# Optimization experiments

Measured on AMD Instinct MI355X. Metric: run time of the kernel, lower is better.

The kernel has to match this reference:

```python
import jax, jax.numpy as jnp
import numpy as np

EPS = 1e-8
DIGIT_TEMPERATURE = 1.0
SEED = 0
B, KMAX, V = 64, 16, 32000
DV, H = 10, 4096
# permute_prob table: prob_table[k] = permute_prob.get(k, 0.0)
_PROB = np.zeros(KMAX + 1, dtype=np.float32)
_PROB[2:] = 0.5
PROB_TABLE = jnp.asarray(_PROB)


def setup_inputs() -> dict:
    key = jax.random.key(0)
    ks = jax.random.split(key, 6)
    p_raw = jax.random.uniform(ks[0], (B, KMAX, V), dtype=jnp.float32)
    p_z = p_raw / p_raw.sum(axis=-1, keepdims=True)  # valid distributions per slot
    return {
        "p_z": p_z,
        "digit_logits_ref": jax.random.normal(ks[1], (B, DV), dtype=jnp.float32),
        "digit_logits_cf": jax.random.normal(ks[2], (B, DV), dtype=jnp.float32),
        "h_ans_ref": jax.random.normal(ks[3], (B, H), dtype=jnp.float32),
        "h_ans_cf": jax.random.normal(ks[4], (B, H), dtype=jnp.float32),
        "k_vals": jax.random.randint(ks[5], (B,), 0, KMAX + 1),
    }


def _js_divergence(p, q, eps=EPS):
    p = jnp.clip(p.astype(jnp.float32), eps)
    q = jnp.clip(q.astype(jnp.float32), eps)
    m = 0.5 * (p + q)
    log_m = jnp.log(m)
    kl_pm = (p * (jnp.log(p) - log_m)).sum(-1)
    kl_qm = (q * (jnp.log(q) - log_m)).sum(-1)
    return 0.5 * (kl_pm + kl_qm)


def _build_counterfactual_pz(p_z, k_vals):
    # Vectorized GS-mode counterfactual: per batch, with prob permute_prob[k]
    # (and k>1) permute the first k slots, otherwise temperature-warp them.
    bsz, kmax, vocab = p_z.shape
    key = jax.random.key(SEED)
    k_dec, k_perm, k_tau = jax.random.split(key, 3)
    u_dec = jax.random.uniform(k_dec, (bsz,))
    do_permute = (k_vals > 1) & (u_dec < PROB_TABLE[k_vals])  # [B]
    slots = jnp.arange(kmax)
    active = slots[None, :] < k_vals[:, None]  # [B, K]
    # ragged permutation of the first k slots: argsort random keys, inactive -> +inf
    u_perm = jax.random.uniform(k_perm, (bsz, kmax))
    perm = jnp.argsort(jnp.where(active, u_perm, jnp.inf), axis=1)  # stable: tail keeps order
    permuted = jnp.take_along_axis(p_z, perm[:, :, None], axis=1)
    # temperature warp: softmax(log(p)/tau), tau ~ U(0.7, 1.6) per slot
    tau = jax.random.uniform(k_tau, (bsz, kmax, 1), minval=0.7, maxval=1.6)
    warped = jax.nn.softmax(jnp.log(jnp.clip(p_z, EPS)) / tau, axis=-1)
    cf = jnp.where(do_permute[:, None, None], permuted, warped)
    return jnp.where(active[:, :, None], cf, p_z)


def reference(p_z, digit_logits_ref, digit_logits_cf, h_ans_ref, h_ans_cf, k_vals):
    p_cf_z = _build_counterfactual_pz(p_z, k_vals)
    # safe_softmax(logits, tau) == softmax(logits / tau)
    p_ref = jax.lax.stop_gradient(
        jax.nn.softmax(digit_logits_ref / DIGIT_TEMPERATURE, axis=-1))
    p_cf = jax.nn.softmax(digit_logits_cf / DIGIT_TEMPERATURE, axis=-1)
    js = _js_divergence(p_ref, p_cf).mean()
    loss_cf = jnp.log(jnp.float32(2.0)) - js
    ref_f = jax.lax.stop_gradient(h_ans_ref.astype(jnp.float32))
    cf_f = h_ans_cf.astype(jnp.float32)
    ref_norm = ref_f / jnp.clip(jnp.linalg.norm(ref_f, axis=-1, keepdims=True), 1e-12)
    cf_norm = cf_f / jnp.clip(jnp.linalg.norm(cf_f, axis=-1, keepdims=True), 1e-12)
    cos_sim = (ref_norm * cf_norm).sum(-1).mean()
    loss_dep = cos_sim - 1.0  # cf_mode == 'gs'
    dep_norm = jnp.linalg.norm(ref_f - cf_f, axis=-1).mean()
    return loss_cf, loss_dep, dep_norm, p_cf_z
```

## Files before the change

kernel.cpp:

```cpp
#include <hip/hip_runtime.h>
#include <stdint.h>

#define NB    64
#define KMAX  16
#define VV    32000
#define DVV   10
#define HH    4096
#define NROWS (NB*KMAX)
#define EPSF  1e-8f
#define NQ    8000

__device__ __forceinline__ uint32_t rotl32(uint32_t v, int r) { return (v << r) | (v >> (32 - r)); }

__device__ __forceinline__ void tf2x32(uint32_t k0, uint32_t k1, uint32_t c0, uint32_t c1,
                                       uint32_t& o0, uint32_t& o1) {
    uint32_t ks2 = k0 ^ k1 ^ 0x1BD11BDAu;
    uint32_t x0 = c0 + k0, x1 = c1 + k1;
    const int RA[4] = {13, 15, 26, 6};
    const int RB[4] = {17, 29, 16, 24};
#pragma unroll
    for (int i = 0; i < 4; ++i) { x0 += x1; x1 = rotl32(x1, RA[i]); x1 ^= x0; }
    x0 += k1; x1 += ks2 + 1u;
#pragma unroll
    for (int i = 0; i < 4; ++i) { x0 += x1; x1 = rotl32(x1, RB[i]); x1 ^= x0; }
    x0 += ks2; x1 += k0 + 2u;
#pragma unroll
    for (int i = 0; i < 4; ++i) { x0 += x1; x1 = rotl32(x1, RA[i]); x1 ^= x0; }
    x0 += k0; x1 += k1 + 3u;
#pragma unroll
    for (int i = 0; i < 4; ++i) { x0 += x1; x1 = rotl32(x1, RB[i]); x1 ^= x0; }
    x0 += k1; x1 += ks2 + 4u;
#pragma unroll
    for (int i = 0; i < 4; ++i) { x0 += x1; x1 = rotl32(x1, RA[i]); x1 ^= x0; }
    x0 += ks2; x1 += k0 + 5u;
    o0 = x0; o1 = x1;
}

__device__ __forceinline__ float bits_to_u01(uint32_t bits) {
    uint32_t fb = (bits >> 9) | 0x3F800000u;
    return __uint_as_float(fb) - 1.0f;
}

__global__ __launch_bounds__(1024) void setup_kernel(const int* __restrict__ k_vals,
                                                     int* __restrict__ src_arr,
                                                     float* __restrict__ itau_arr) {
    const int j = threadIdx.x;
    const int b = j >> 4, s = j & 15;

    __shared__ float su[NROWS];
    __shared__ int   sk[NB];
    __shared__ int   sdp[NB];

    uint32_t a0, b0, a1, b1, a2, b2;
    tf2x32(0u, 0u, 0u, 3u, a0, b0);
    tf2x32(0u, 0u, 1u, 4u, a1, b1);
    tf2x32(0u, 0u, 2u, 5u, a2, b2);
    const uint32_t kdec0 = a0, kdec1 = a1;
    const uint32_t kperm0 = a2, kperm1 = b0;
    const uint32_t ktau0 = b1, ktau1 = b2;

    uint32_t y0, y1, pb, tb;
    if (j < 512) { tf2x32(kperm0, kperm1, (uint32_t)j, (uint32_t)(j + 512), y0, y1); pb = y0; }
    else         { tf2x32(kperm0, kperm1, (uint32_t)(j - 512), (uint32_t)j, y0, y1); pb = y1; }
    su[j] = bits_to_u01(pb);
    if (j < 512) { tf2x32(ktau0, ktau1, (uint32_t)j, (uint32_t)(j + 512), y0, y1); tb = y0; }
    else         { tf2x32(ktau0, ktau1, (uint32_t)(j - 512), (uint32_t)j, y0, y1); tb = y1; }
    float tau = fmaxf(0.7f, bits_to_u01(tb) * 0.9f + 0.7f);
    float itau = 1.0f / tau;

    if (j < NB) {
        uint32_t bits;
        if (j < 32) { tf2x32(kdec0, kdec1, (uint32_t)j, (uint32_t)(j + 32), y0, y1); bits = y0; }
        else        { tf2x32(kdec0, kdec1, (uint32_t)(j - 32), (uint32_t)j, y0, y1); bits = y1; }
        float u_dec = bits_to_u01(bits);
        int k = k_vals[j];
        float prob = (k >= 2) ? 0.5f : 0.0f;
        sk[j] = k;
        sdp[j] = (k > 1) && (u_dec < prob);
    }
    __syncthreads();

    const int k = sk[b];
    const bool dp = sdp[b] != 0;
    const float INF = __int_as_float(0x7F800000);
    const float myk = (s < k) ? su[j] : INF;

    int r = 0;
#pragma unroll
    for (int t = 0; t < KMAX; ++t) {
        float kt = (t < k) ? su[(b << 4) + t] : INF;
        r += (kt < myk) || (kt == myk && t < s);
    }

    if (s >= k)      { src_arr[j] = s;            itau_arr[j] = 0.0f; }
    else if (dp)     { src_arr[(b << 4) + r] = s; itau_arr[(b << 4) + r] = 0.0f; }
    else             { src_arr[j] = -1;           itau_arr[j] = itau; }
}

__global__ __launch_bounds__(256) void rowred_kernel(const float* __restrict__ hr,
                                                     const float* __restrict__ hc,
                                                     float* __restrict__ cosb,
                                                     float* __restrict__ depb) {
    int b = blockIdx.x;
    const float4* r4 = (const float4*)(hr + (size_t)b * HH);
    const float4* c4 = (const float4*)(hc + (size_t)b * HH);
    float srr = 0.f, scc = 0.f, sxc = 0.f, sdd = 0.f;
    for (int i = threadIdx.x; i < HH / 4; i += 256) {
        float4 r = r4[i], c = c4[i];
        srr += r.x * r.x + r.y * r.y + r.z * r.z + r.w * r.w;
        scc += c.x * c.x + c.y * c.y + c.z * c.z + c.w * c.w;
        sxc += r.x * c.x + r.y * c.y + r.z * c.z + r.w * c.w;
        float dx = r.x - c.x, dy = r.y - c.y, dz = r.z - c.z, dw = r.w - c.w;
        sdd += dx * dx + dy * dy + dz * dz + dw * dw;
    }
#pragma unroll
    for (int o = 32; o; o >>= 1) {
        srr += __shfl_down(srr, o, 64);
        scc += __shfl_down(scc, o, 64);
        sxc += __shfl_down(sxc, o, 64);
        sdd += __shfl_down(sdd, o, 64);
    }
    __shared__ float red[4][4];
    int w = threadIdx.x >> 6;
    if ((threadIdx.x & 63) == 0) { red[w][0] = srr; red[w][1] = scc; red[w][2] = sxc; red[w][3] = sdd; }
    __syncthreads();
    if (threadIdx.x == 0) {
        float t0 = 0.f, t1 = 0.f, t2 = 0.f, t3 = 0.f;
        for (int i = 0; i < 4; ++i) { t0 += red[i][0]; t1 += red[i][1]; t2 += red[i][2]; t3 += red[i][3]; }
        float nr = fmaxf(sqrtf(t0), 1e-12f);
        float nc = fmaxf(sqrtf(t1), 1e-12f);
        cosb[b] = t2 / (nr * nc);
        depb[b] = sqrtf(t3);
    }
}

__global__ void finalize_kernel(const float* __restrict__ dlr, const float* __restrict__ dlc,
                                const float* __restrict__ cosb, const float* __restrict__ depb,
                                float* __restrict__ out) {
    int b = threadIdx.x;
    float lr[DVV], lc[DVV];
    float mr = -1e30f, mc = -1e30f;
#pragma unroll
    for (int v = 0; v < DVV; ++v) {
        lr[v] = dlr[b * DVV + v]; lc[v] = dlc[b * DVV + v];
        mr = fmaxf(mr, lr[v]); mc = fmaxf(mc, lc[v]);
    }
    float sr = 0.f, sc = 0.f;
#pragma unroll
    for (int v = 0; v < DVV; ++v) {
        lr[v] = expf(lr[v] - mr); sr += lr[v];
        lc[v] = expf(lc[v] - mc); sc += lc[v];
    }
    float js = 0.f;
#pragma unroll
    for (int v = 0; v < DVV; ++v) {
        float p = fmaxf(lr[v] / sr, EPSF);
        float q = fmaxf(lc[v] / sc, EPSF);
        float m = 0.5f * (p + q);
        float lm = logf(m);
        js += 0.5f * (p * (logf(p) - lm) + q * (logf(q) - lm));
    }
    float cs = cosb[b], dp = depb[b];
#pragma unroll
    for (int o = 32; o; o >>= 1) {
        js += __shfl_down(js, o, 64);
        cs += __shfl_down(cs, o, 64);
        dp += __shfl_down(dp, o, 64);
    }
    if (b == 0) {
        out[0] = logf(2.0f) - js * (1.0f / 64.0f);
        out[1] = cs * (1.0f / 64.0f) - 1.0f;
        out[2] = dp * (1.0f / 64.0f);
    }
}

__global__ __launch_bounds__(1024) void cf_main_kernel(const float* __restrict__ p_z,
                                                       const int* __restrict__ src_arr,
                                                       const float* __restrict__ itau_arr,
                                                       float* __restrict__ out) {
    const int row = blockIdx.x;
    const int b = row >> 4;
    const int src = src_arr[row];
    const int tid = threadIdx.x;
    const int lane = tid & 63;
    float* dst = out + (size_t)row * VV;

    if (src >= 0) {
        const float* s = p_z + ((size_t)((b << 4) + src)) * VV;
#pragma unroll
        for (int i = 0; i < 8; ++i) {
            const int q = tid + (i << 10);
            if (q >= NQ) break;
            float4 v = *(const float4*)(s + (q << 2));
            float nx = __shfl_down(v.x, 1, 64);
            if (q < NQ - 1) {
                float4 st;
                st.x = v.y; st.y = v.z; st.z = v.w;
                st.w = (lane == 63) ? s[(q << 2) + 4] : nx;
                *(float4*)(dst + (q << 2) + 1) = st;
            }
            if (q == 0) dst[0] = v.x;
            if (q == NQ - 1) { dst[VV - 3] = v.y; dst[VV - 2] = v.z; dst[VV - 1] = v.w; }
        }
        return;
    }

    const float it = itau_arr[row];
    const float* s = p_z + (size_t)row * VV;
    float4 r[8];
    float lsum = 0.f;
#pragma unroll
    for (int i = 0; i < 8; ++i) {
        const int q = tid + (i << 10);
        if (q < NQ) {
            float4 v = *(const float4*)(s + (q << 2));
            v.x = exp2f(__log2f(fmaxf(v.x, EPSF)) * it);
            v.y = exp2f(__log2f(fmaxf(v.y, EPSF)) * it);
            v.z = exp2f(__log2f(fmaxf(v.z, EPSF)) * it);
            v.w = exp2f(__log2f(fmaxf(v.w, EPSF)) * it);
            r[i] = v;
            lsum += v.x + v.y + v.z + v.w;
        } else {
            r[i] = make_float4(0.f, 0.f, 0.f, 0.f);
        }
    }
    __shared__ float red[16];
    float t = lsum;
#pragma unroll
    for (int o = 32; o; o >>= 1) t += __shfl_down(t, o, 64);
    if (lane == 0) red[tid >> 6] = t;
    __syncthreads();
    if (tid < 64) {
        float u = (tid < 16) ? red[tid] : 0.0f;
#pragma unroll
        for (int o = 8; o; o >>= 1) u += __shfl_down(u, o, 64);
        if (tid == 0) red[0] = u;
    }
    __syncthreads();
    const float scale = 1.0f / red[0];

#pragma unroll
    for (int i = 0; i < 8; ++i) {
        const int q = tid + (i << 10);
        if (q >= NQ) break;
        float nx = __shfl_down(r[i].x, 1, 64);
        if (q < NQ - 1) {
            float4 st;
            st.x = r[i].y * scale; st.y = r[i].z * scale; st.z = r[i].w * scale;
            if (lane == 63)
                nx = exp2f(__log2f(fmaxf(s[(q << 2) + 4], EPSF)) * it);
            st.w = nx * scale;
            *(float4*)(dst + (q << 2) + 1) = st;
        }
        if (q == 0) dst[0] = r[i].x * scale;
        if (q == NQ - 1) {
            dst[VV - 3] = r[i].y * scale;
            dst[VV - 2] = r[i].z * scale;
            dst[VV - 1] = r[i].w * scale;
        }
    }
}

extern "C" void kernel_launch(void* const* d_in, const int* in_sizes, int n_in,
                              void* d_out, int out_size, void* d_ws, size_t ws_size,
                              hipStream_t stream) {
    const float* p_z = (const float*)d_in[0];
    const float* dlr = (const float*)d_in[1];
    const float* dlc = (const float*)d_in[2];
    const float* hr  = (const float*)d_in[3];
    const float* hc  = (const float*)d_in[4];
    const int*   kv  = (const int*)d_in[5];
    float* out = (float*)d_out;

    int*   src_arr  = (int*)d_ws;
    float* itau_arr = (float*)d_ws + NROWS;
    float* cosb     = (float*)d_ws + 2 * NROWS;
    float* depb     = cosb + NB;

    setup_kernel<<<1, 1024, 0, stream>>>(kv, src_arr, itau_arr);
    cf_main_kernel<<<NROWS, 1024, 0, stream>>>(p_z, src_arr, itau_arr, out + 3);
    rowred_kernel<<<NB, 256, 0, stream>>>(hr, hc, cosb, depb);
    finalize_kernel<<<1, 64, 0, stream>>>(dlr, dlc, cosb, depb, out);
}
```

Measured before the change: 62.64 us.

## Split warp normalization into row-sum pass and flat grid-stride output kernel

Replaces the one-block-per-row counterfactual kernel with two kernels. The first computes the per-row softmax normalization for warped rows. The second is a flat grid-stride kernel that writes aligned float4 stores across the whole output, with offsets handled per element group. This removes the shuffles and register-held rows of the old kernel and gives an even, row-independent workload. The cost is reading warped rows twice and doing a per-group integer division and extra branching.

```diff
diff --git a/kernel.cpp b/kernel.cpp
--- a/kernel.cpp
+++ b/kernel.cpp
@@ -9,6 +9,8 @@
 #define NROWS (NB*KMAX)
 #define EPSF  1e-8f
 #define NQ    8000
+#define TOTELEM (NROWS*VV)
+#define TGROUPS ((TOTELEM - 4) / 4)
 
 __device__ __forceinline__ uint32_t rotl32(uint32_t v, int r) { return (v << r) | (v >> (32 - r)); }
 
@@ -95,6 +97,84 @@
     if (s >= k)      { src_arr[j] = s;            itau_arr[j] = 0.0f; }
     else if (dp)     { src_arr[(b << 4) + r] = s; itau_arr[(b << 4) + r] = 0.0f; }
     else             { src_arr[j] = -1;           itau_arr[j] = itau; }
+}
+
+__global__ __launch_bounds__(256) void rowsum_kernel(const float* __restrict__ p_z,
+                                                     const int* __restrict__ src_arr,
+                                                     const float* __restrict__ itau_arr,
+                                                     float* __restrict__ scale_arr) {
+    const int row = blockIdx.x;
+    const int tid = threadIdx.x;
+    if (src_arr[row] >= 0) { if (tid == 0) scale_arr[row] = 1.0f; return; }
+    const float it = itau_arr[row];
+    const float* s = p_z + (size_t)row * VV;
+    float lsum = 0.f;
+    for (int i = tid; i < NQ; i += 256) {
+        float4 v = *(const float4*)(s + (i << 2));
+        lsum += exp2f(__log2f(fmaxf(v.x, EPSF)) * it)
+              + exp2f(__log2f(fmaxf(v.y, EPSF)) * it)
+              + exp2f(__log2f(fmaxf(v.z, EPSF)) * it)
+              + exp2f(__log2f(fmaxf(v.w, EPSF)) * it);
+    }
+#pragma unroll
+    for (int o = 32; o; o >>= 1) lsum += __shfl_down(lsum, o, 64);
+    __shared__ float red[4];
+    if ((tid & 63) == 0) red[tid >> 6] = lsum;
+    __syncthreads();
+    if (tid == 0) scale_arr[row] = 1.0f / (red[0] + red[1] + red[2] + red[3]);
+}
+
+__device__ __forceinline__ float cf_elem(const float* __restrict__ p_z,
+                                         const int* __restrict__ src_arr,
+                                         const float* __restrict__ itau_arr,
+                                         const float* __restrict__ scale_arr,
+                                         uint32_t row, uint32_t v) {
+    int src = src_arr[row];
+    if (src >= 0) return p_z[(size_t)((row & ~15u) + (uint32_t)src) * VV + v];
+    float p = fmaxf(p_z[(size_t)row * VV + v], EPSF);
+    return exp2f(__log2f(p) * itau_arr[row]) * scale_arr[row];
+}
+
+__global__ __launch_bounds__(256) void cf_flat_kernel(const float* __restrict__ p_z,
+                                                      const int* __restrict__ src_arr,
+                                                      const float* __restrict__ itau_arr,
+                                                      const float* __restrict__ scale_arr,
+                                                      float* __restrict__ o ) {
+    const uint32_t stride = gridDim.x * blockDim.x;
+    for (uint32_t t = blockIdx.x * blockDim.x + threadIdx.x; t < TGROUPS; t += stride) {
+        const uint32_t e0 = 4u * t + 1u;
+        const uint32_t row = e0 / VV;
+        const uint32_t v0 = e0 - row * VV;
+        float4 stv;
+        if (v0 != VV - 3) {
+            const int src = src_arr[row];
+            if (src >= 0) {
+                const float* s = p_z + (size_t)((row & ~15u) + (uint32_t)src) * VV + v0;
+                stv = *(const float4*)s;
+            } else {
+                const float it = itau_arr[row];
+                const float sc = scale_arr[row];
+                const float* s = p_z + (size_t)row * VV + v0;
+                float4 v = *(const float4*)s;
+                stv.x = exp2f(__log2f(fmaxf(v.x, EPSF)) * it) * sc;
+                stv.y = exp2f(__log2f(fmaxf(v.y, EPSF)) * it) * sc;
+                stv.z = exp2f(__log2f(fmaxf(v.z, EPSF)) * it) * sc;
+                stv.w = exp2f(__log2f(fmaxf(v.w, EPSF)) * it) * sc;
+            }
+        } else {
+            stv.x = cf_elem(p_z, src_arr, itau_arr, scale_arr, row, VV - 3);
+            stv.y = cf_elem(p_z, src_arr, itau_arr, scale_arr, row, VV - 2);
+            stv.z = cf_elem(p_z, src_arr, itau_arr, scale_arr, row, VV - 1);
+            stv.w = cf_elem(p_z, src_arr, itau_arr, scale_arr, row + 1, 0);
+        }
+        *(float4*)(o + 3 + e0) = stv;
+    }
+    if (blockIdx.x == 0 && threadIdx.x == 0) {
+        o[3] = cf_elem(p_z, src_arr, itau_arr, scale_arr, 0, 0);
+        o[3 + TOTELEM - 3] = cf_elem(p_z, src_arr, itau_arr, scale_arr, NROWS - 1, VV - 3);
+        o[3 + TOTELEM - 2] = cf_elem(p_z, src_arr, itau_arr, scale_arr, NROWS - 1, VV - 2);
+        o[3 + TOTELEM - 1] = cf_elem(p_z, src_arr, itau_arr, scale_arr, NROWS - 1, VV - 1);
+    }
 }
 
 __global__ __launch_bounds__(256) void rowred_kernel(const float* __restrict__ hr,
@@ -174,93 +254,6 @@
     }
 }
 
-__global__ __launch_bounds__(1024) void cf_main_kernel(const float* __restrict__ p_z,
-                                                       const int* __restrict__ src_arr,
-                                                       const float* __restrict__ itau_arr,
-                                                       float* __restrict__ out) {
-    const int row = blockIdx.x;
-    const int b = row >> 4;
-    const int src = src_arr[row];
-    const int tid = threadIdx.x;
-    const int lane = tid & 63;
-    float* dst = out + (size_t)row * VV;
-
-    if (src >= 0) {
-        const float* s = p_z + ((size_t)((b << 4) + src)) * VV;
-#pragma unroll
-        for (int i = 0; i < 8; ++i) {
-            const int q = tid + (i << 10);
-            if (q >= NQ) break;
-            float4 v = *(const float4*)(s + (q << 2));
-            float nx = __shfl_down(v.x, 1, 64);
-            if (q < NQ - 1) {
-                float4 st;
-                st.x = v.y; st.y = v.z; st.z = v.w;
-                st.w = (lane == 63) ? s[(q << 2) + 4] : nx;
-                *(float4*)(dst + (q << 2) + 1) = st;
-            }
-            if (q == 0) dst[0] = v.x;
-            if (q == NQ - 1) { dst[VV - 3] = v.y; dst[VV - 2] = v.z; dst[VV - 1] = v.w; }
-        }
-        return;
-    }
-
-    const float it = itau_arr[row];
-    const float* s = p_z + (size_t)row * VV;
-    float4 r[8];
-    float lsum = 0.f;
-#pragma unroll
-    for (int i = 0; i < 8; ++i) {
-        const int q = tid + (i << 10);
-        if (q < NQ) {
-            float4 v = *(const float4*)(s + (q << 2));
-            v.x = exp2f(__log2f(fmaxf(v.x, EPSF)) * it);
-            v.y = exp2f(__log2f(fmaxf(v.y, EPSF)) * it);
-            v.z = exp2f(__log2f(fmaxf(v.z, EPSF)) * it);
-            v.w = exp2f(__log2f(fmaxf(v.w, EPSF)) * it);
-            r[i] = v;
-            lsum += v.x + v.y + v.z + v.w;
-        } else {
-            r[i] = make_float4(0.f, 0.f, 0.f, 0.f);
-        }
-    }
-    __shared__ float red[16];
-    float t = lsum;
-#pragma unroll
-    for (int o = 32; o; o >>= 1) t += __shfl_down(t, o, 64);
-    if (lane == 0) red[tid >> 6] = t;
-    __syncthreads();
-    if (tid < 64) {
-        float u = (tid < 16) ? red[tid] : 0.0f;
-#pragma unroll
-        for (int o = 8; o; o >>= 1) u += __shfl_down(u, o, 64);
-        if (tid == 0) red[0] = u;
-    }
-    __syncthreads();
-    const float scale = 1.0f / red[0];
-
-#pragma unroll
-    for (int i = 0; i < 8; ++i) {
-        const int q = tid + (i << 10);
-        if (q >= NQ) break;
-        float nx = __shfl_down(r[i].x, 1, 64);
-        if (q < NQ - 1) {
-            float4 st;
-            st.x = r[i].y * scale; st.y = r[i].z * scale; st.z = r[i].w * scale;
-            if (lane == 63)
-                nx = exp2f(__log2f(fmaxf(s[(q << 2) + 4], EPSF)) * it);
-            st.w = nx * scale;
-            *(float4*)(dst + (q << 2) + 1) = st;
-        }
-        if (q == 0) dst[0] = r[i].x * scale;
-        if (q == NQ - 1) {
-            dst[VV - 3] = r[i].y * scale;
-            dst[VV - 2] = r[i].z * scale;
-            dst[VV - 1] = r[i].w * scale;
-        }
-    }
-}
-
 extern "C" void kernel_launch(void* const* d_in, const int* in_sizes, int n_in,
                               void* d_out, int out_size, void* d_ws, size_t ws_size,
                               hipStream_t stream) {
@@ -272,13 +265,15 @@
     const int*   kv  = (const int*)d_in[5];
     float* out = (float*)d_out;
 
-    int*   src_arr  = (int*)d_ws;
-    float* itau_arr = (float*)d_ws + NROWS;
-    float* cosb     = (float*)d_ws + 2 * NROWS;
-    float* depb     = cosb + NB;
+    int*   src_arr   = (int*)d_ws;
+    float* itau_arr  = (float*)d_ws + NROWS;
+    float* scale_arr = (float*)d_ws + 2 * NROWS;
+    float* cosb      = (float*)d_ws + 3 * NROWS;
+    float* depb      = cosb + NB;
 
     setup_kernel<<<1, 1024, 0, stream>>>(kv, src_arr, itau_arr);
-    cf_main_kernel<<<NROWS, 1024, 0, stream>>>(p_z, src_arr, itau_arr, out + 3);
+    rowsum_kernel<<<NROWS, 256, 0, stream>>>(p_z, src_arr, itau_arr, scale_arr);
+    cf_flat_kernel<<<4096, 256, 0, stream>>>(p_z, src_arr, itau_arr, scale_arr, out);
     rowred_kernel<<<NB, 256, 0, stream>>>(hr, hc, cosb, depb);
     finalize_kernel<<<1, 64, 0, stream>>>(dlr, dlc, cosb, depb, out);
 }
```

Measured after the change: 75.87 us. +21.1%, slower.
